# Performance work log

Measured on AMD Instinct MI355X. Metric: run time of the kernel, lower is better.

Reference implementation:

```python
import jax, jax.numpy as jnp
import numpy as np

IN_FEATURES = 512
OUT_FEATURES = 512
GRID_MIN = -2.0
GRID_MAX = 2.0
NUM_GRIDS = 8
SPLINE_SCALE = 0.1
BATCH = 16384


def setup_inputs() -> dict:
    key = jax.random.key(0)
    kx, kw = jax.random.split(key)
    x = jax.random.normal(kx, (BATCH, IN_FEATURES), dtype=jnp.float32)
    grid = jnp.linspace(GRID_MIN, GRID_MAX, NUM_GRIDS, dtype=jnp.float32)
    spline_weight = (
        jax.random.normal(kw, (IN_FEATURES * NUM_GRIDS, OUT_FEATURES), dtype=jnp.float32)
        * SPLINE_SCALE
    )
    return {"x": x, "grid": grid, "spline_weight": spline_weight}


def reference(x, grid, spline_weight):
    # denominator h = (grid_max - grid_min) / (num_grids - 1)
    h = (GRID_MAX - GRID_MIN) / (NUM_GRIDS - 1)
    # basis: [B, in_features, num_grids]
    basis = jnp.exp(-jnp.square((x[..., None] - grid) / h))
    # flatten to [B, in_features * num_grids] and GEMM
    return basis.reshape(basis.shape[0], -1) @ spline_weight
```

## Files before the change

### kernel.cpp

```cpp
#include <hip/hip_runtime.h>
#include <hip/hip_bf16.h>

#define BATCH 16384
#define IN_F 512
#define OUT_F 512
#define NG 8
#define KTOT (IN_F * NG)

#define SH    2.1019642153762872f
#define SSTEP 1.2011224087864498f
#define BC0N  4.2039284307525745f
#define RC1   2.4022448175728996f

typedef __attribute__((ext_vector_type(8))) short short8;
typedef __attribute__((ext_vector_type(4))) float f32x4;
typedef __attribute__((ext_vector_type(2))) float f32x2;
typedef __attribute__((ext_vector_type(4))) unsigned int u32x4;
typedef __attribute__((ext_vector_type(2))) unsigned int u32x2;

__device__ __forceinline__ unsigned fbits(float f) {
    union { float f; unsigned u; } v; v.f = f; return v.u;
}
__device__ __forceinline__ unsigned pack2bf(float lo, float hi) {
    return __builtin_amdgcn_perm(fbits(hi) + 0x8000u, fbits(lo) + 0x8000u,
                                 0x07060302u);
}
__device__ __forceinline__ unsigned cvtpk(float lo, float hi) {
    unsigned r;
    asm("v_cvt_pk_bf16_f32 %0, %1, %2" : "=v"(r) : "v"(lo), "v"(hi));
    return r;
}

__device__ __forceinline__ void lds_barrier() {
    __asm__ volatile("" ::: "memory");
    __builtin_amdgcn_sched_barrier(0);
    __builtin_amdgcn_s_waitcnt(0xC07F);
    __builtin_amdgcn_s_barrier();
    __builtin_amdgcn_sched_barrier(0);
    __asm__ volatile("" ::: "memory");
}

__global__ void wt_swizzle(const float* __restrict__ W, unsigned short* __restrict__ Wt) {
    const int gid  = blockIdx.x * 256 + threadIdx.x;
    const int lane = gid & 63;
    const int f    = (gid >> 6) & 7;
    const int kt   = (gid >> 9) & 63;
    const int s    = gid >> 15;
    const int j  = f & 3, kk = f >> 2;
    const int l15 = lane & 15, lq = lane >> 4;
    const int n  = s * 64 + j * 16 + l15;
    const int k0 = kt * 64 + kk * 32 + lq * 8;
    constexpr float QS[8] = {1.0f,
                             3.6787944117144233e-1f,
                             1.8315638888734179e-2f,
                             1.2340980408667956e-4f,
                             1.1253517471925912e-7f,
                             1.3887943864964021e-11f,
                             2.3195228302435693e-16f,
                             5.2428856633634640e-22f};
    u32x4 pk;
#pragma unroll
    for (int e = 0; e < 4; ++e)
        pk[e] = pack2bf(W[(size_t)(k0 + 2 * e) * OUT_F + n] * QS[2 * e],
                        W[(size_t)(k0 + 2 * e + 1) * OUT_F + n] * QS[2 * e + 1]);
    *(u32x4*)(Wt + (size_t)gid * 8) = pk;
}

__global__ __launch_bounds__(256, 4) void gauss_gemm13(
        const float* __restrict__ X, const unsigned short* __restrict__ Wt,
        float* __restrict__ Out) {
    __shared__ __align__(16) unsigned short sA[4 * 4096];

    const int tid  = threadIdx.x;
    const int lane = tid & 63;
    const int wave = tid >> 6;
    const int nb = (blockIdx.x & 7) * 128 + (blockIdx.x >> 3);
    const int cb = nb >> 8;
    const int rb = nb & 255;
    const int m0 = rb * 64;
    const int l15 = lane & 15;
    const int lq  = lane >> 4;
    const int s   = cb * 2 + (wave >> 1);
    const int jo  = (wave & 1) * 2;

    const int aw0 = lane * 64 + (((2 * wave)     ^ (lane & 7)) << 3);
    const int aw1 = lane * 64 + (((2 * wave + 1) ^ (lane & 7)) << 3);
    const float* xlp = X + (size_t)(m0 + lane) * IN_F + wave * 2;

    int aofs[2][4];
#pragma unroll
    for (int kk = 0; kk < 2; ++kk)
#pragma unroll
        for (int i = 0; i < 4; ++i)
            aofs[kk][i] = (i * 16 + l15) * 64 + (((kk * 4 + lq) ^ (l15 & 7)) << 3);

    const unsigned short* bptr = Wt + (size_t)s * 262144 + lane * 8;

    f32x4 acc[4][2];
#pragma unroll
    for (int i = 0; i < 4; ++i)
#pragma unroll
        for (int j = 0; j < 2; ++j)
            acc[i][j] = (f32x4){0.f, 0.f, 0.f, 0.f};

    auto stageA = [&](f32x2 xv, int slot) {
        unsigned short* base = sA + slot * 4096;
#pragma unroll
        for (int h = 0; h < 2; ++h) {
            const float t0  = fmaf(h ? xv.y : xv.x, SH, BC0N);
            const float rho = __builtin_amdgcn_exp2f(t0 * RC1);
            const float v0  = __builtin_amdgcn_exp2f(-t0 * t0);
            const float v1 = v0 * rho;
            const float v2 = v1 * rho;
            const float v3 = v2 * rho;
            const float v4 = v3 * rho;
            const float v5 = v4 * rho;
            const float v6 = v5 * rho;
            const float v7 = v6 * rho;
            u32x4 pk;
            pk[0] = cvtpk(v0, v1);
            pk[1] = cvtpk(v2, v3);
            pk[2] = cvtpk(v4, v5);
            pk[3] = cvtpk(v6, v7);
            *(u32x4*)(base + (h ? aw1 : aw0)) = pk;
        }
    };

    short8 bfA[4], bfB[4];
    f32x2 xu, xv;

    {
        f32x2 x0 = *(const f32x2*)(xlp);
        f32x2 x1 = *(const f32x2*)(xlp + 8);
        xu = *(const f32x2*)(xlp + 16);
        xv = *(const f32x2*)(xlp + 24);
#pragma unroll
        for (int q = 0; q < 4; ++q)
            bfA[q] = *(const short8*)(bptr + ((q >> 1) * 4 + jo + (q & 1)) * 512);
        stageA(x0, 0);
        stageA(x1, 1);
        lds_barrier();
    }

#define GG13(KT, SLOT, BU, BF, XUSE)                                           \
    {                                                                          \
        const int kn1 = ((KT) + 1 < 64) ? (KT) + 1 : 63;                       \
        const int kn4 = ((KT) + 4 < 64) ? (KT) + 4 : 63;                       \
        _Pragma("unroll")                                                      \
        for (int q = 0; q < 4; ++q)                                            \
            BF[q] = *(const short8*)(bptr + (size_t)kn1 * 4096 +               \
                                     ((q >> 1) * 4 + jo + (q & 1)) * 512);     \
        short8 af[2][4];                                                       \
        _Pragma("unroll")                                                      \
        for (int kk = 0; kk < 2; ++kk)                                         \
            _Pragma("unroll")                                                  \
            for (int i = 0; i < 4; ++i)                                        \
                af[kk][i] = *(const short8*)(sA + (SLOT) * 4096 + aofs[kk][i]);\
        stageA(XUSE, (SLOT) ^ 2);                                              \
        XUSE = *(const f32x2*)(xlp + (size_t)kn4 * 8);                         \
        __builtin_amdgcn_s_setprio(1);                                         \
        _Pragma("unroll")                                                      \
        for (int kk = 0; kk < 2; ++kk)                                         \
            _Pragma("unroll")                                                  \
            for (int i = 0; i < 4; ++i)                                        \
                _Pragma("unroll")                                              \
                for (int j = 0; j < 2; ++j)                                    \
                    acc[i][j] = __builtin_amdgcn_mfma_f32_16x16x32_bf16(       \
                        af[kk][i], BU[kk * 2 + j], acc[i][j], 0, 0, 0);        \
        __builtin_amdgcn_s_setprio(0);                                         \
        if (((SLOT) & 1) == 1) lds_barrier();                                  \
    }

    for (int kt0 = 0; kt0 < 64; kt0 += 4) {
        GG13(kt0 + 0, 0, bfA, bfB, xu)
        GG13(kt0 + 1, 1, bfB, bfA, xv)
        GG13(kt0 + 2, 2, bfA, bfB, xu)
        GG13(kt0 + 3, 3, bfB, bfA, xv)
    }
#undef GG13

#pragma unroll
    for (int i = 0; i < 4; ++i) {
        const int r0 = m0 + i * 16 + lq * 4;
#pragma unroll
        for (int j = 0; j < 2; ++j) {
            const int c = cb * 128 + wave * 32 + j * 16 + l15;
#pragma unroll
            for (int e = 0; e < 4; ++e)
                Out[(size_t)(r0 + e) * OUT_F + c] = acc[i][j][e];
        }
    }
}

#define BM 128
#define BN 128
#define BK 64
#define LDA 72
#define LDB 72

__global__ __launch_bounds__(256, 2) void gauss_gemm_fb(
        const float* __restrict__ X, const float* __restrict__ W,
        float* __restrict__ Out) {
    __shared__ __align__(16) unsigned short sA[BM * LDA];
    __shared__ __align__(16) unsigned short sB2[BN * LDB];

    const int tid  = threadIdx.x;
    const int lane = tid & 63;
    const int wave = tid >> 6;
    const int rb = blockIdx.x >> 2;
    const int cbx = blockIdx.x & 3;
    const int m0 = rb * BM;
    const int n0 = cbx * BN;
    const int wr = (wave >> 1) * 64;
    const int wc = (wave & 1) * 64;
    const int l15 = lane & 15;
    const int lq  = lane >> 4;

    f32x4 acc[4][4];
#pragma unroll
    for (int i = 0; i < 4; ++i)
#pragma unroll
        for (int j = 0; j < 4; ++j)
            acc[i][j] = (f32x4){0.f, 0.f, 0.f, 0.f};

    const int arow = tid & 127;
    const int axq  = tid >> 7;

    for (int kt = 0; kt < KTOT / BK; ++kt) {
        const int k0  = kt * BK;
        const int xc0 = kt * (BK / NG);

        const f32x4 xv = *(const f32x4*)(X + (size_t)(m0 + arow) * IN_F + xc0 + 4 * axq);
        unsigned short* sArow = sA + arow * LDA + axq * 32;
#pragma unroll
        for (int j = 0; j < 4; ++j) {
            const float xs = xv[j] * SH;
            u32x4 pk;
#pragma unroll
            for (int g = 0; g < 8; g += 2) {
                float t0 = xs + (BC0N - g * SSTEP);
                float t1 = xs + (BC0N - (g + 1) * SSTEP);
                pk[g >> 1] = pack2bf(__builtin_amdgcn_exp2f(-t0 * t0),
                                     __builtin_amdgcn_exp2f(-t1 * t1));
            }
            *(u32x4*)(sArow + j * 8) = pk;
        }

#pragma unroll
        for (int p = 0; p < 8; ++p) {
            int id = p * 256 + tid;
            int n  = id & 127;
            int k4 = id >> 7;
            const float* wp = W + (size_t)(k0 + k4 * 4) * OUT_F + n0 + n;
            u32x2 v;
            v[0] = pack2bf(wp[0], wp[OUT_F]);
            v[1] = pack2bf(wp[2 * OUT_F], wp[3 * OUT_F]);
            *(u32x2*)(sB2 + n * LDB + k4 * 4) = v;
        }

        __syncthreads();

#pragma unroll
        for (int kk = 0; kk < BK; kk += 32) {
            short8 af[4], bfv[4];
#pragma unroll
            for (int i = 0; i < 4; ++i)
                af[i] = *(const short8*)(sA + (wr + i * 16 + l15) * LDA + kk + lq * 8);
#pragma unroll
            for (int i = 0; i < 4; ++i)
                bfv[i] = *(const short8*)(sB2 + (wc + i * 16 + l15) * LDB + kk + lq * 8);
#pragma unroll
            for (int i = 0; i < 4; ++i)
#pragma unroll
                for (int j = 0; j < 4; ++j)
                    acc[i][j] = __builtin_amdgcn_mfma_f32_16x16x32_bf16(af[i], bfv[j], acc[i][j], 0, 0, 0);
        }

        __syncthreads();
    }

#pragma unroll
    for (int i = 0; i < 4; ++i) {
        const int r0 = m0 + wr + i * 16 + lq * 4;
#pragma unroll
        for (int j = 0; j < 4; ++j) {
            const int c = n0 + wc + j * 16 + l15;
#pragma unroll
            for (int e = 0; e < 4; ++e)
                Out[(size_t)(r0 + e) * OUT_F + c] = acc[i][j][e];
        }
    }
}

extern "C" void kernel_launch(void* const* d_in, const int* in_sizes, int n_in,
                              void* d_out, int out_size, void* d_ws, size_t ws_size,
                              hipStream_t stream) {
    (void)in_sizes; (void)n_in; (void)out_size;
    const float* X = (const float*)d_in[0];
    const float* W = (const float*)d_in[2];
    float* Out = (float*)d_out;

    const size_t wt_bytes = (size_t)KTOT * OUT_F * sizeof(unsigned short);
    if (ws_size >= wt_bytes) {
        unsigned short* Wt = (unsigned short*)d_ws;
        wt_swizzle<<<dim3(KTOT * OUT_F / 8 / 256), 256, 0, stream>>>(W, Wt);
        gauss_gemm13<<<dim3((BATCH / 64) * (OUT_F / 128)), 256, 0, stream>>>(X, Wt, Out);
    } else {
        gauss_gemm_fb<<<dim3((BATCH / BM) * (OUT_F / BN)), 256, 0, stream>>>(X, W, Out);
    }
}
```

Before: 166.5 us.

## Widen GEMM block to 512 threads covering 256 output columns per tile

Doubles the workgroup to 8 waves so each 64-row block covers 256 output columns instead of 128. Each wave now computes Gaussian basis values for one input feature per k-step rather than two, which halves the redundant per-block basis generation relative to the MFMA work. The LDS ring grows from 4 to 8 slots, and the x prefetch distance changes to match. The rho power chain is shortened with rho squared, and packing uses the HIP bf16 intrinsic instead of inline asm. The cost is twice the LDS per block and larger barriers, which may lower occupancy.

```diff
diff --git a/kernel.cpp b/kernel.cpp
--- a/kernel.cpp
+++ b/kernel.cpp
@@ -24,11 +24,6 @@
 __device__ __forceinline__ unsigned pack2bf(float lo, float hi) {
     return __builtin_amdgcn_perm(fbits(hi) + 0x8000u, fbits(lo) + 0x8000u,
                                  0x07060302u);
-}
-__device__ __forceinline__ unsigned cvtpk(float lo, float hi) {
-    unsigned r;
-    asm("v_cvt_pk_bf16_f32 %0, %1, %2" : "=v"(r) : "v"(lo), "v"(hi));
-    return r;
 }
 
 __device__ __forceinline__ void lds_barrier() {
@@ -66,26 +61,25 @@
     *(u32x4*)(Wt + (size_t)gid * 8) = pk;
 }
 
-__global__ __launch_bounds__(256, 4) void gauss_gemm13(
+__global__ __launch_bounds__(512, 4) void gauss_gemm17(
         const float* __restrict__ X, const unsigned short* __restrict__ Wt,
         float* __restrict__ Out) {
-    __shared__ __align__(16) unsigned short sA[4 * 4096];
+    __shared__ __align__(16) unsigned short sA[8 * 4096];
 
     const int tid  = threadIdx.x;
     const int lane = tid & 63;
     const int wave = tid >> 6;
-    const int nb = (blockIdx.x & 7) * 128 + (blockIdx.x >> 3);
+    const int nb = (blockIdx.x & 7) * 64 + (blockIdx.x >> 3);
     const int cb = nb >> 8;
     const int rb = nb & 255;
     const int m0 = rb * 64;
     const int l15 = lane & 15;
     const int lq  = lane >> 4;
-    const int s   = cb * 2 + (wave >> 1);
+    const int s   = cb * 4 + (wave >> 1);
     const int jo  = (wave & 1) * 2;
 
-    const int aw0 = lane * 64 + (((2 * wave)     ^ (lane & 7)) << 3);
-    const int aw1 = lane * 64 + (((2 * wave + 1) ^ (lane & 7)) << 3);
-    const float* xlp = X + (size_t)(m0 + lane) * IN_F + wave * 2;
+    const int aw = lane * 64 + ((wave ^ (lane & 7)) << 3);
+    const float* xlp = X + (size_t)(m0 + lane) * IN_F + wave;
 
     int aofs[2][4];
 #pragma unroll
@@ -103,49 +97,48 @@
         for (int j = 0; j < 2; ++j)
             acc[i][j] = (f32x4){0.f, 0.f, 0.f, 0.f};
 
-    auto stageA = [&](f32x2 xv, int slot) {
-        unsigned short* base = sA + slot * 4096;
-#pragma unroll
-        for (int h = 0; h < 2; ++h) {
-            const float t0  = fmaf(h ? xv.y : xv.x, SH, BC0N);
-            const float rho = __builtin_amdgcn_exp2f(t0 * RC1);
-            const float v0  = __builtin_amdgcn_exp2f(-t0 * t0);
-            const float v1 = v0 * rho;
-            const float v2 = v1 * rho;
-            const float v3 = v2 * rho;
-            const float v4 = v3 * rho;
-            const float v5 = v4 * rho;
-            const float v6 = v5 * rho;
-            const float v7 = v6 * rho;
-            u32x4 pk;
-            pk[0] = cvtpk(v0, v1);
-            pk[1] = cvtpk(v2, v3);
-            pk[2] = cvtpk(v4, v5);
-            pk[3] = cvtpk(v6, v7);
-            *(u32x4*)(base + (h ? aw1 : aw0)) = pk;
-        }
+    auto stageA = [&](float x, int slot) {
+        const float t0  = fmaf(x, SH, BC0N);
+        const float rho = __builtin_amdgcn_exp2f(t0 * RC1);
+        const float v0  = __builtin_amdgcn_exp2f(-t0 * t0);
+        const float r2  = rho * rho;
+        const float v1 = v0 * rho;
+        const float v2 = v0 * r2, v3 = v1 * r2;
+        const float v4 = v2 * r2, v5 = v3 * r2;
+        const float v6 = v4 * r2, v7 = v5 * r2;
+        union { __hip_bfloat162 h[4]; u32x4 u; } pk;
+        pk.h[0] = __float22bfloat162_rn(make_float2(v0, v1));
+        pk.h[1] = __float22bfloat162_rn(make_float2(v2, v3));
+        pk.h[2] = __float22bfloat162_rn(make_float2(v4, v5));
+        pk.h[3] = __float22bfloat162_rn(make_float2(v6, v7));
+        *(u32x4*)(sA + slot * 4096 + aw) = pk.u;
     };
 
     short8 bfA[4], bfB[4];
-    f32x2 xu, xv;
+    float xu, xv;
 
     {
-        f32x2 x0 = *(const f32x2*)(xlp);
-        f32x2 x1 = *(const f32x2*)(xlp + 8);
-        xu = *(const f32x2*)(xlp + 16);
-        xv = *(const f32x2*)(xlp + 24);
+        const float x0 = xlp[0];
+        const float x1 = xlp[8];
+        const float x2 = xlp[16];
+        const float x3 = xlp[24];
+        xu = xlp[32];
+        xv = xlp[40];
 #pragma unroll
         for (int q = 0; q < 4; ++q)
             bfA[q] = *(const short8*)(bptr + ((q >> 1) * 4 + jo + (q & 1)) * 512);
         stageA(x0, 0);
         stageA(x1, 1);
+        stageA(x2, 2);
+        stageA(x3, 3);
         lds_barrier();
     }
 
-#define GG13(KT, SLOT, BU, BF, XUSE)                                           \
+#define GG17(KT0, S, BU, BF, XUSE)                                             \
     {                                                                          \
-        const int kn1 = ((KT) + 1 < 64) ? (KT) + 1 : 63;                       \
-        const int kn4 = ((KT) + 4 < 64) ? (KT) + 4 : 63;                       \
+        const int kt  = (KT0) + (S);                                           \
+        const int kn1 = (kt + 1 < 64) ? kt + 1 : 63;                           \
+        const int kn6 = (kt + 6 < 64) ? kt + 6 : 63;                           \
         _Pragma("unroll")                                                      \
         for (int q = 0; q < 4; ++q)                                            \
             BF[q] = *(const short8*)(bptr + (size_t)kn1 * 4096 +               \
@@ -155,9 +148,9 @@
         for (int kk = 0; kk < 2; ++kk)                                         \
             _Pragma("unroll")                                                  \
             for (int i = 0; i < 4; ++i)                                        \
-                af[kk][i] = *(const short8*)(sA + (SLOT) * 4096 + aofs[kk][i]);\
-        stageA(XUSE, (SLOT) ^ 2);                                              \
-        XUSE = *(const f32x2*)(xlp + (size_t)kn4 * 8);                         \
+                af[kk][i] = *(const short8*)(sA + (S) * 4096 + aofs[kk][i]);   \
+        stageA(XUSE, ((S) + 4) & 7);                                           \
+        XUSE = xlp[(size_t)kn6 * 8];                                           \
         __builtin_amdgcn_s_setprio(1);                                         \
         _Pragma("unroll")                                                      \
         for (int kk = 0; kk < 2; ++kk)                                         \
@@ -168,23 +161,27 @@
                     acc[i][j] = __builtin_amdgcn_mfma_f32_16x16x32_bf16(       \
                         af[kk][i], BU[kk * 2 + j], acc[i][j], 0, 0, 0);        \
         __builtin_amdgcn_s_setprio(0);                                         \
-        if (((SLOT) & 1) == 1) lds_barrier();                                  \
-    }
-
-    for (int kt0 = 0; kt0 < 64; kt0 += 4) {
-        GG13(kt0 + 0, 0, bfA, bfB, xu)
-        GG13(kt0 + 1, 1, bfB, bfA, xv)
-        GG13(kt0 + 2, 2, bfA, bfB, xu)
-        GG13(kt0 + 3, 3, bfB, bfA, xv)
-    }
-#undef GG13
+        if (((S) & 3) == 3) lds_barrier();                                     \
+    }
+
+    for (int kt0 = 0; kt0 < 64; kt0 += 8) {
+        GG17(kt0, 0, bfA, bfB, xu)
+        GG17(kt0, 1, bfB, bfA, xv)
+        GG17(kt0, 2, bfA, bfB, xu)
+        GG17(kt0, 3, bfB, bfA, xv)
+        GG17(kt0, 4, bfA, bfB, xu)
+        GG17(kt0, 5, bfB, bfA, xv)
+        GG17(kt0, 6, bfA, bfB, xu)
+        GG17(kt0, 7, bfB, bfA, xv)
+    }
+#undef GG17
 
 #pragma unroll
     for (int i = 0; i < 4; ++i) {
         const int r0 = m0 + i * 16 + lq * 4;
 #pragma unroll
         for (int j = 0; j < 2; ++j) {
-            const int c = cb * 128 + wave * 32 + j * 16 + l15;
+            const int c = cb * 256 + (wave >> 1) * 64 + (jo + j) * 16 + l15;
 #pragma unroll
             for (int e = 0; e < 4; ++e)
                 Out[(size_t)(r0 + e) * OUT_F + c] = acc[i][j][e];
@@ -304,7 +301,7 @@
     if (ws_size >= wt_bytes) {
         unsigned short* Wt = (unsigned short*)d_ws;
         wt_swizzle<<<dim3(KTOT * OUT_F / 8 / 256), 256, 0, stream>>>(W, Wt);
-        gauss_gemm13<<<dim3((BATCH / 64) * (OUT_F / 128)), 256, 0, stream>>>(X, Wt, Out);
+        gauss_gemm17<<<dim3((BATCH / 64) * (OUT_F / 256)), 512, 0, stream>>>(X, Wt, Out);
     } else {
         gauss_gemm_fb<<<dim3((BATCH / BM) * (OUT_F / BN)), 256, 0, stream>>>(X, W, Out);
     }
```

Result: faster. 161.8 us (-2.8%).
